# Kernel tuning notes

Hardware: AMD Instinct MI355X
Metric: run time of the kernel (lower is better)

The kernel has to match this reference:

```python
import jax, jax.numpy as jnp
import numpy as np


def setup_inputs() -> dict:
    key = jax.random.key(0)
    k1, k2 = jax.random.split(key)
    x = jax.random.normal(k1, (8, 2500, 100), dtype=jnp.float32)          # [B, L, E]
    label_feature = jax.random.normal(k2, (8922, 100), dtype=jnp.float32)  # [N, E]
    return {"x": x, "label_feature": label_feature}


def reference(x, label_feature):
    # scores: [B, N, L] = label_feature @ x^T (broadcast query over batch), unscaled
    scores = jnp.einsum("ne,ble->bnl", label_feature, x)
    alpha = jax.nn.softmax(scores, axis=2)  # softmax over sequence length
    # m: [B, N, E] = alpha @ x
    m = jnp.einsum("bnl,ble->bne", alpha, x)
    return m
```

## Files before the change

### kernel.cpp

```cpp
#include <hip/hip_runtime.h>
#include <math.h>
#include <stdint.h>

typedef __attribute__((ext_vector_type(8))) _Float16 half8;
typedef __attribute__((ext_vector_type(4))) _Float16 half4;
typedef __attribute__((ext_vector_type(4))) float f32x4;

constexpr int Bb = 8, Ll = 2500, Ee = 100, Nn = 8922;
constexpr int LP = 2560, EP = 128, NP = 8960;
constexpr int LT = 64;
constexpr int NTILES = LP / LT;
constexpr int NTB = 128;

constexpr size_t SZ_LF = (size_t)NP * EP * 2;
constexpr size_t SZ_XW = (size_t)Bb * LP * EP * 2;
constexpr size_t OFF_XW = SZ_LF;
constexpr size_t OFF_XT = OFF_XW + SZ_XW;
constexpr size_t WS_NEED = OFF_XT + SZ_XW;

__device__ __forceinline__ void gload16(const void* g, void* l) {
    __builtin_amdgcn_global_load_lds(
        (const __attribute__((address_space(1))) uint32_t*)g,
        (__attribute__((address_space(3))) uint32_t*)l, 16, 0, 0);
}

__global__ __launch_bounds__(256)
void prep_lf(const float* __restrict__ lf, uint32_t* __restrict__ dst) {
    int idx = blockIdx.x * 256 + threadIdx.x;
    int n = idx >> 6, ep = idx & 63;
    int e0 = 2 * ep, e1 = e0 + 1;
    float f0 = (n < Nn && e0 < Ee) ? lf[(size_t)n * Ee + e0] : 0.f;
    float f1 = (n < Nn && e1 < Ee) ? lf[(size_t)n * Ee + e1] : (e1 == 127 ? 1.0f : 0.f);
    union { _Float16 h[2]; uint32_t u; } cv;
    cv.h[0] = (_Float16)f0; cv.h[1] = (_Float16)f1;
    dst[idx] = cv.u;
}

__global__ __launch_bounds__(256)
void prep_x(const float* __restrict__ x, uint32_t* __restrict__ dxw,
            uint16_t* __restrict__ dxt) {
    __shared__ float lx[LT][101];
    const int l0 = blockIdx.x * LT;
    const int b  = blockIdx.y;
    for (int i = threadIdx.x; i < LT * Ee; i += 256) {
        int ll = i / Ee, e = i - ll * Ee;
        int l = l0 + ll;
        lx[ll][e] = (l < Ll) ? x[((size_t)b * Ll + l) * Ee + e] : 0.f;
    }
    __syncthreads();
    for (int i = threadIdx.x; i < LT * 64; i += 256) {
        int row = i >> 6, ep = i & 63;
        int l = l0 + row;
        int e0 = 2 * ep, e1 = e0 + 1;
        float f0 = (e0 < Ee) ? lx[row][e0] : 0.f;
        float f1;
        if (e1 < Ee)        f1 = lx[row][e1];
        else if (e1 == 127) f1 = (l < Ll) ? 0.f : -20000.f;
        else                f1 = 0.f;
        union { _Float16 h[2]; uint32_t u; } cv;
        cv.h[0] = (_Float16)f0; cv.h[1] = (_Float16)f1;
        int boff = (4 * ep) ^ ((row & 7) << 4);
        dxw[((size_t)b * LP + l) * 64 + (boff >> 2)] = cv.u;
    }
    for (int i = threadIdx.x; i < EP * LT; i += 256) {
        int e = i >> 6, ll = i & 63;
        float v = (e < Ee) ? lx[ll][e] : 0.f;
        uint32_t boff = (uint32_t)((2 * ll) ^ ((e & 7) << 4));
        union { _Float16 h; uint16_t u; } cv; cv.h = (_Float16)v;
        dxt[((size_t)b * EP + e) * LP + l0 + (boff >> 1)] = cv.u;
    }
}

__global__ __launch_bounds__(256, 2)
void cwa_mfma(const uint16_t* __restrict__ lf16, const uint16_t* __restrict__ xw,
              const uint16_t* __restrict__ xt, float* __restrict__ out) {
    __shared__ __align__(128) char smem[2 * 32768 + 4 * 4096];
    const int tid = threadIdx.x, lane = tid & 63, w = tid >> 6;
    const int g = lane >> 4, nl = lane & 15;
    const int b = blockIdx.y;
    const int n_base = blockIdx.x * NTB + w * 32;

    half8 qf[2][4];
#pragma unroll
    for (int nh = 0; nh < 2; nh++) {
        const uint16_t* qr = lf16 + (size_t)(n_base + 16 * nh + nl) * EP + 8 * g;
#pragma unroll
        for (int ks = 0; ks < 4; ks++) qf[nh][ks] = *(const half8*)(qr + 32 * ks);
    }

    f32x4 oacc[2][7];
#pragma unroll
    for (int nh = 0; nh < 2; nh++)
#pragma unroll
        for (int es = 0; es < 7; es++) oacc[nh][es] = f32x4{0.f, 0.f, 0.f, 0.f};
    float m_i[2] = {-INFINITY, -INFINITY}, s_i[2] = {0.f, 0.f};

    const char* xwb = (const char*)(xw + (size_t)b * LP * EP);
    const char* xtb = (const char*)(xt + (size_t)b * EP * LP);

    auto stage = [&](int t, char* kbuf) {
        const char* kg = xwb + (size_t)t * LT * EP * 2;
        const char* vg = xtb + (size_t)t * LT * 2;
        char* vbuf = kbuf + 16384;
#pragma unroll
        for (int i = 0; i < 4; i++) {
            int uo = i * 4096 + w * 1024;
            gload16(kg + uo + lane * 16, kbuf + uo);
        }
#pragma unroll
        for (int i = 0; i < 4; i++) {
            int e0 = w * 32 + i * 8;
            gload16(vg + (size_t)(e0 + (lane >> 3)) * (LP * 2) + (lane & 7) * 16,
                    vbuf + e0 * 128);
        }
    };

    stage(0, smem);
    asm volatile("s_waitcnt vmcnt(0)" ::: "memory");
    __syncthreads();

    char* pb = smem + 65536 + w * 4096;
    const int swp = (nl & 7) << 4;

    for (int t = 0; t < NTILES; t++) {
        const int buf = t & 1;
        const char* kb = smem + buf * 32768;
        const char* vb = kb + 16384;

        if (t + 1 < NTILES) stage(t + 1, smem + (buf ^ 1) * 32768);

        f32x4 sacc[2][4];
#pragma unroll
        for (int nh = 0; nh < 2; nh++)
#pragma unroll
            for (int ls = 0; ls < 4; ls++) sacc[nh][ls] = f32x4{0.f, 0.f, 0.f, 0.f};
#pragma unroll
        for (int ls = 0; ls < 4; ls++) {
            const int lrow = 16 * ls + nl;
            const char* kr = kb + lrow * 256;
            const int sw = (lrow & 7) << 4;
#pragma unroll
            for (int ks = 0; ks < 4; ks++) {
                half8 kf = *(const half8*)(kr + ((64 * ks + 16 * g) ^ sw));
                sacc[0][ls] = __builtin_amdgcn_mfma_f32_16x16x32_f16(kf, qf[0][ks], sacc[0][ls], 0, 0, 0);
                sacc[1][ls] = __builtin_amdgcn_mfma_f32_16x16x32_f16(kf, qf[1][ks], sacc[1][ls], 0, 0, 0);
            }
        }

        float scale_s[2];
        half4 ph[2][4];
#pragma unroll
        for (int nh = 0; nh < 2; nh++) {
            float tm = -INFINITY;
#pragma unroll
            for (int ls = 0; ls < 4; ls++)
#pragma unroll
                for (int r = 0; r < 4; r++) tm = fmaxf(tm, sacc[nh][ls][r]);
            tm = fmaxf(tm, __shfl_xor(tm, 16, 64));
            tm = fmaxf(tm, __shfl_xor(tm, 32, 64));
            const float mn = fmaxf(m_i[nh], tm);
            scale_s[nh] = __expf(m_i[nh] - mn);
            float ts = 0.f;
#pragma unroll
            for (int ls = 0; ls < 4; ls++)
#pragma unroll
                for (int r = 0; r < 4; r++) {
                    float pv = __expf(sacc[nh][ls][r] - mn);
                    ts += pv;
                    ph[nh][ls][r] = (_Float16)pv;
                }
            ts += __shfl_xor(ts, 16, 64);
            ts += __shfl_xor(ts, 32, 64);
            s_i[nh] = s_i[nh] * scale_s[nh] + ts;
            m_i[nh] = mn;
        }

#pragma unroll
        for (int nh = 0; nh < 2; nh++)
#pragma unroll
            for (int r = 0; r < 4; r++) {
                float scr = __shfl(scale_s[nh], 4 * g + r, 64);
#pragma unroll
                for (int es = 0; es < 7; es++) oacc[nh][es][r] *= scr;
            }

#pragma unroll
        for (int nh = 0; nh < 2; nh++)
#pragma unroll
            for (int ls = 0; ls < 4; ls++)
                *(half4*)(pb + (16 * nh + nl) * 128 + ((32 * ls + 8 * g) ^ swp)) = ph[nh][ls];

#pragma unroll
        for (int kl = 0; kl < 2; kl++) {
            half8 pf0 = *(const half8*)(pb + nl * 128 + ((64 * kl + 16 * g) ^ swp));
            half8 pf1 = *(const half8*)(pb + (16 + nl) * 128 + ((64 * kl + 16 * g) ^ swp));
#pragma unroll
            for (int es = 0; es < 7; es++) {
                const int er = 16 * es + nl;
                half8 vf = *(const half8*)(vb + er * 128 + ((64 * kl + 16 * g) ^ ((er & 7) << 4)));
                oacc[0][es] = __builtin_amdgcn_mfma_f32_16x16x32_f16(pf0, vf, oacc[0][es], 0, 0, 0);
                oacc[1][es] = __builtin_amdgcn_mfma_f32_16x16x32_f16(pf1, vf, oacc[1][es], 0, 0, 0);
            }
        }

        asm volatile("s_waitcnt vmcnt(0)" ::: "memory");
        __syncthreads();
    }

#pragma unroll
    for (int nh = 0; nh < 2; nh++) {
        const float inv = 1.0f / s_i[nh];
#pragma unroll
        for (int r = 0; r < 4; r++) {
            const float invr = __shfl(inv, 4 * g + r, 64);
            const int n = n_base + 16 * nh + 4 * g + r;
            if (n < Nn) {
#pragma unroll
                for (int es = 0; es < 7; es++) {
                    const int e = 16 * es + nl;
                    if (e < Ee) out[((size_t)b * Nn + n) * Ee + e] = oacc[nh][es][r] * invr;
                }
            }
        }
    }
}

constexpr int FNT = 16, FLT = 64, FLTP = 65;
__global__ __launch_bounds__(256)
void cwa_fwd(const float* __restrict__ x, const float* __restrict__ lf,
             float* __restrict__ out) {
    __shared__ float q[FNT][Ee];
    __shared__ float xts[Ee][FLTP];
    __shared__ float pl[FNT][FLT];
    const int tid = threadIdx.x, lane = tid & 63, w = tid >> 6;
    const int b = blockIdx.y, n0 = blockIdx.x * FNT;
    for (int idx = tid; idx < FNT * Ee; idx += 256) {
        int nl = idx / Ee, e = idx - nl * Ee;
        int n = n0 + nl;
        q[nl][e] = (n < Nn) ? lf[n * Ee + e] : 0.0f;
    }
    float m_i[4], s_i[4], a0[4], a1[4];
#pragma unroll
    for (int i = 0; i < 4; i++) { m_i[i] = -INFINITY; s_i[i] = 0.f; a0[i] = 0.f; a1[i] = 0.f; }
    const float* xb = x + (size_t)b * Ll * Ee;
    const bool hi_ok = lane < (Ee - 64);
    for (int l0 = 0; l0 < Ll; l0 += FLT) {
        const int nrows = min(FLT, Ll - l0);
        __syncthreads();
        for (int idx = tid; idx < FLT * (Ee / 4); idx += 256) {
            int r = idx / (Ee / 4), c4 = idx - r * (Ee / 4);
            float4 v = make_float4(0.f, 0.f, 0.f, 0.f);
            if (r < nrows) v = *reinterpret_cast<const float4*>(xb + (size_t)(l0 + r) * Ee + c4 * 4);
            xts[c4 * 4 + 0][r] = v.x; xts[c4 * 4 + 1][r] = v.y;
            xts[c4 * 4 + 2][r] = v.z; xts[c4 * 4 + 3][r] = v.w;
        }
        __syncthreads();
        float sc[4] = {0.f, 0.f, 0.f, 0.f};
        for (int e = 0; e < Ee; e++) {
            float xv = xts[e][lane];
#pragma unroll
            for (int i = 0; i < 4; i++) sc[i] = fmaf(q[4 * w + i][e], xv, sc[i]);
        }
        const bool valid = lane < nrows;
#pragma unroll
        for (int i = 0; i < 4; i++) {
            float s = valid ? sc[i] : -INFINITY;
            float tm = s;
#pragma unroll
            for (int msk = 32; msk >= 1; msk >>= 1) tm = fmaxf(tm, __shfl_xor(tm, msk, 64));
            float mn = fmaxf(m_i[i], tm);
            float p = __expf(s - mn);
            float sm = p;
#pragma unroll
            for (int msk = 32; msk >= 1; msk >>= 1) sm += __shfl_xor(sm, msk, 64);
            float scl = __expf(m_i[i] - mn);
            s_i[i] = s_i[i] * scl + sm; m_i[i] = mn;
            a0[i] *= scl; a1[i] *= scl;
            pl[4 * w + i][lane] = p;
        }
        __syncthreads();
#pragma unroll 4
        for (int l = 0; l < FLT; l++) {
            float xv0 = xts[lane][l];
            float xv1 = hi_ok ? xts[64 + lane][l] : 0.f;
#pragma unroll
            for (int i = 0; i < 4; i++) {
                float pv = pl[4 * w + i][l];
                a0[i] = fmaf(pv, xv0, a0[i]); a1[i] = fmaf(pv, xv1, a1[i]);
            }
        }
    }
#pragma unroll
    for (int i = 0; i < 4; i++) {
        int n = n0 + 4 * w + i;
        if (n >= Nn) continue;
        float inv = 1.0f / s_i[i];
        size_t base = ((size_t)b * Nn + n) * Ee;
        out[base + lane] = a0[i] * inv;
        if (hi_ok) out[base + 64 + lane] = a1[i] * inv;
    }
}

extern "C" void kernel_launch(void* const* d_in, const int* in_sizes, int n_in,
                              void* d_out, int out_size, void* d_ws, size_t ws_size,
                              hipStream_t stream) {
    const float* x  = (const float*)d_in[0];
    const float* lf = (const float*)d_in[1];
    float* out = (float*)d_out;
    if (ws_size >= WS_NEED) {
        prep_lf<<<NP * 64 / 256, 256, 0, stream>>>(lf, (uint32_t*)d_ws);
        prep_x<<<dim3(LP / LT, Bb), 256, 0, stream>>>(
            x, (uint32_t*)((char*)d_ws + OFF_XW), (uint16_t*)((char*)d_ws + OFF_XT));
        cwa_mfma<<<dim3(NP / NTB, Bb), 256, 0, stream>>>(
            (const uint16_t*)d_ws, (const uint16_t*)((char*)d_ws + OFF_XW),
            (const uint16_t*)((char*)d_ws + OFF_XT), out);
    } else {
        dim3 grid((Nn + FNT - 1) / FNT, Bb);
        cwa_fwd<<<grid, dim3(256), 0, stream>>>(x, lf, out);
    }
}
```

Baseline: 248.3 us.

## Shrink L tile to 32, raise occupancy, and add lazy softmax rescaling

Halves the sequence tile in the flash-style attention kernel, shrinking shared memory from about 80KB to 40KB and raising the launch-bounds occupancy hint from 2 to 4 blocks per CU. The V-transpose swizzle and the P scratch layout are reworked for 64-byte rows. Online softmax now rescales the accumulators only when some wave's new max exceeds the running max by more than 8, which skips most rescale work. In exchange there are twice as many loop iterations and barriers, fewer MFMAs per tile to hide latency, and a register cap that could cause spills.

```diff
diff --git a/kernel.cpp b/kernel.cpp
--- a/kernel.cpp
+++ b/kernel.cpp
@@ -8,7 +8,7 @@
 
 constexpr int Bb = 8, Ll = 2500, Ee = 100, Nn = 8922;
 constexpr int LP = 2560, EP = 128, NP = 8960;
-constexpr int LT = 64;
+constexpr int LT = 32;
 constexpr int NTILES = LP / LT;
 constexpr int NTB = 128;
 
@@ -39,16 +39,16 @@
 __global__ __launch_bounds__(256)
 void prep_x(const float* __restrict__ x, uint32_t* __restrict__ dxw,
             uint16_t* __restrict__ dxt) {
-    __shared__ float lx[LT][101];
-    const int l0 = blockIdx.x * LT;
+    __shared__ float lx[64][101];
+    const int l0 = blockIdx.x * 64;
     const int b  = blockIdx.y;
-    for (int i = threadIdx.x; i < LT * Ee; i += 256) {
+    for (int i = threadIdx.x; i < 64 * Ee; i += 256) {
         int ll = i / Ee, e = i - ll * Ee;
         int l = l0 + ll;
         lx[ll][e] = (l < Ll) ? x[((size_t)b * Ll + l) * Ee + e] : 0.f;
     }
     __syncthreads();
-    for (int i = threadIdx.x; i < LT * 64; i += 256) {
+    for (int i = threadIdx.x; i < 64 * 64; i += 256) {
         int row = i >> 6, ep = i & 63;
         int l = l0 + row;
         int e0 = 2 * ep, e1 = e0 + 1;
@@ -62,19 +62,19 @@
         int boff = (4 * ep) ^ ((row & 7) << 4);
         dxw[((size_t)b * LP + l) * 64 + (boff >> 2)] = cv.u;
     }
-    for (int i = threadIdx.x; i < EP * LT; i += 256) {
+    for (int i = threadIdx.x; i < EP * 64; i += 256) {
         int e = i >> 6, ll = i & 63;
         float v = (e < Ee) ? lx[ll][e] : 0.f;
-        uint32_t boff = (uint32_t)((2 * ll) ^ ((e & 7) << 4));
+        uint32_t boff = (uint32_t)((2 * ll) ^ ((e & 3) << 4));
         union { _Float16 h; uint16_t u; } cv; cv.h = (_Float16)v;
         dxt[((size_t)b * EP + e) * LP + l0 + (boff >> 1)] = cv.u;
     }
 }
 
-__global__ __launch_bounds__(256, 2)
+__global__ __launch_bounds__(256, 4)
 void cwa_mfma(const uint16_t* __restrict__ lf16, const uint16_t* __restrict__ xw,
               const uint16_t* __restrict__ xt, float* __restrict__ out) {
-    __shared__ __align__(128) char smem[2 * 32768 + 4 * 4096];
+    __shared__ __align__(128) char smem[16384 + 16384 + 8192];
     const int tid = threadIdx.x, lane = tid & 63, w = tid >> 6;
     const int g = lane >> 4, nl = lane & 15;
     const int b = blockIdx.y;
@@ -98,44 +98,45 @@
     const char* xwb = (const char*)(xw + (size_t)b * LP * EP);
     const char* xtb = (const char*)(xt + (size_t)b * EP * LP);
 
-    auto stage = [&](int t, char* kbuf) {
+    auto stage = [&](int t, int par) {
+        char* kbuf = smem + par * 8192;
+        char* vbuf = smem + 16384 + par * 8192;
         const char* kg = xwb + (size_t)t * LT * EP * 2;
         const char* vg = xtb + (size_t)t * LT * 2;
-        char* vbuf = kbuf + 16384;
-#pragma unroll
-        for (int i = 0; i < 4; i++) {
-            int uo = i * 4096 + w * 1024;
-            gload16(kg + uo + lane * 16, kbuf + uo);
-        }
-#pragma unroll
-        for (int i = 0; i < 4; i++) {
-            int e0 = w * 32 + i * 8;
-            gload16(vg + (size_t)(e0 + (lane >> 3)) * (LP * 2) + (lane & 7) * 16,
-                    vbuf + e0 * 128);
+#pragma unroll
+        for (int i = 0; i < 2; i++) {
+            int off = i * 4096 + w * 1024 + lane * 16;
+            gload16(kg + off, kbuf + off);
+        }
+#pragma unroll
+        for (int i = 0; i < 2; i++) {
+            int erow = i * 64 + w * 16 + (lane >> 2);
+            gload16(vg + (size_t)erow * (LP * 2) + (lane & 3) * 16,
+                    vbuf + i * 4096 + w * 1024 + lane * 16);
         }
     };
 
-    stage(0, smem);
+    stage(0, 0);
     asm volatile("s_waitcnt vmcnt(0)" ::: "memory");
     __syncthreads();
 
-    char* pb = smem + 65536 + w * 4096;
-    const int swp = (nl & 7) << 4;
+    char* pb = smem + 32768 + w * 2048;
+    const int swp = (nl & 3) << 4;
 
     for (int t = 0; t < NTILES; t++) {
-        const int buf = t & 1;
-        const char* kb = smem + buf * 32768;
-        const char* vb = kb + 16384;
-
-        if (t + 1 < NTILES) stage(t + 1, smem + (buf ^ 1) * 32768);
-
-        f32x4 sacc[2][4];
+        const int par = t & 1;
+        const char* kb = smem + par * 8192;
+        const char* vb = smem + 16384 + par * 8192;
+
+        if (t + 1 < NTILES) stage(t + 1, par ^ 1);
+
+        f32x4 sacc[2][2];
 #pragma unroll
         for (int nh = 0; nh < 2; nh++)
 #pragma unroll
-            for (int ls = 0; ls < 4; ls++) sacc[nh][ls] = f32x4{0.f, 0.f, 0.f, 0.f};
-#pragma unroll
-        for (int ls = 0; ls < 4; ls++) {
+            for (int ls = 0; ls < 2; ls++) sacc[nh][ls] = f32x4{0.f, 0.f, 0.f, 0.f};
+#pragma unroll
+        for (int ls = 0; ls < 2; ls++) {
             const int lrow = 16 * ls + nl;
             const char* kr = kb + lrow * 256;
             const int sw = (lrow & 7) << 4;
@@ -147,57 +148,62 @@
             }
         }
 
-        float scale_s[2];
-        half4 ph[2][4];
+        float tm[2];
 #pragma unroll
         for (int nh = 0; nh < 2; nh++) {
-            float tm = -INFINITY;
-#pragma unroll
-            for (int ls = 0; ls < 4; ls++)
-#pragma unroll
-                for (int r = 0; r < 4; r++) tm = fmaxf(tm, sacc[nh][ls][r]);
-            tm = fmaxf(tm, __shfl_xor(tm, 16, 64));
-            tm = fmaxf(tm, __shfl_xor(tm, 32, 64));
-            const float mn = fmaxf(m_i[nh], tm);
-            scale_s[nh] = __expf(m_i[nh] - mn);
+            float a0 = fmaxf(fmaxf(sacc[nh][0][0], sacc[nh][0][1]),
+                             fmaxf(sacc[nh][0][2], sacc[nh][0][3]));
+            float a1 = fmaxf(fmaxf(sacc[nh][1][0], sacc[nh][1][1]),
+                             fmaxf(sacc[nh][1][2], sacc[nh][1][3]));
+            float tmv = fmaxf(a0, a1);
+            tmv = fmaxf(tmv, __shfl_xor(tmv, 16, 64));
+            tmv = fmaxf(tmv, __shfl_xor(tmv, 32, 64));
+            tm[nh] = tmv;
+        }
+
+        if (!__all((tm[0] <= m_i[0] + 8.f) && (tm[1] <= m_i[1] + 8.f))) {
+#pragma unroll
+            for (int nh = 0; nh < 2; nh++) {
+                const float mn = fmaxf(m_i[nh], tm[nh]);
+                const float sc = __expf(m_i[nh] - mn);
+                m_i[nh] = mn;
+                s_i[nh] *= sc;
+#pragma unroll
+                for (int r = 0; r < 4; r++) {
+                    float scr = __shfl(sc, 4 * g + r, 64);
+#pragma unroll
+                    for (int es = 0; es < 7; es++) oacc[nh][es][r] *= scr;
+                }
+            }
+        }
+
+#pragma unroll
+        for (int nh = 0; nh < 2; nh++) {
             float ts = 0.f;
-#pragma unroll
-            for (int ls = 0; ls < 4; ls++)
+            half4 ph[2];
+#pragma unroll
+            for (int ls = 0; ls < 2; ls++)
 #pragma unroll
                 for (int r = 0; r < 4; r++) {
-                    float pv = __expf(sacc[nh][ls][r] - mn);
+                    float pv = __expf(sacc[nh][ls][r] - m_i[nh]);
                     ts += pv;
-                    ph[nh][ls][r] = (_Float16)pv;
+                    ph[ls][r] = (_Float16)pv;
                 }
             ts += __shfl_xor(ts, 16, 64);
             ts += __shfl_xor(ts, 32, 64);
-            s_i[nh] = s_i[nh] * scale_s[nh] + ts;
-            m_i[nh] = mn;
-        }
-
-#pragma unroll
-        for (int nh = 0; nh < 2; nh++)
-#pragma unroll
-            for (int r = 0; r < 4; r++) {
-                float scr = __shfl(scale_s[nh], 4 * g + r, 64);
-#pragma unroll
-                for (int es = 0; es < 7; es++) oacc[nh][es][r] *= scr;
-            }
-
-#pragma unroll
-        for (int nh = 0; nh < 2; nh++)
-#pragma unroll
-            for (int ls = 0; ls < 4; ls++)
-                *(half4*)(pb + (16 * nh + nl) * 128 + ((32 * ls + 8 * g) ^ swp)) = ph[nh][ls];
-
-#pragma unroll
-        for (int kl = 0; kl < 2; kl++) {
-            half8 pf0 = *(const half8*)(pb + nl * 128 + ((64 * kl + 16 * g) ^ swp));
-            half8 pf1 = *(const half8*)(pb + (16 + nl) * 128 + ((64 * kl + 16 * g) ^ swp));
+            s_i[nh] += ts;
+#pragma unroll
+            for (int ls = 0; ls < 2; ls++)
+                *(half4*)(pb + (16 * nh + nl) * 64 + ((32 * ls + 8 * g) ^ swp)) = ph[ls];
+        }
+
+        {
+            half8 pf0 = *(const half8*)(pb + nl * 64 + ((16 * g) ^ swp));
+            half8 pf1 = *(const half8*)(pb + (16 + nl) * 64 + ((16 * g) ^ swp));
 #pragma unroll
             for (int es = 0; es < 7; es++) {
                 const int er = 16 * es + nl;
-                half8 vf = *(const half8*)(vb + er * 128 + ((64 * kl + 16 * g) ^ ((er & 7) << 4)));
+                half8 vf = *(const half8*)(vb + er * 64 + ((16 * g) ^ ((er & 3) << 4)));
                 oacc[0][es] = __builtin_amdgcn_mfma_f32_16x16x32_f16(pf0, vf, oacc[0][es], 0, 0, 0);
                 oacc[1][es] = __builtin_amdgcn_mfma_f32_16x16x32_f16(pf1, vf, oacc[1][es], 0, 0, 0);
             }
@@ -265,10 +271,10 @@
 #pragma unroll
         for (int i = 0; i < 4; i++) {
             float s = valid ? sc[i] : -INFINITY;
-            float tm = s;
-#pragma unroll
-            for (int msk = 32; msk >= 1; msk >>= 1) tm = fmaxf(tm, __shfl_xor(tm, msk, 64));
-            float mn = fmaxf(m_i[i], tm);
+            float tmv = s;
+#pragma unroll
+            for (int msk = 32; msk >= 1; msk >>= 1) tmv = fmaxf(tmv, __shfl_xor(tmv, msk, 64));
+            float mn = fmaxf(m_i[i], tmv);
             float p = __expf(s - mn);
             float sm = p;
 #pragma unroll
@@ -309,7 +315,7 @@
     float* out = (float*)d_out;
     if (ws_size >= WS_NEED) {
         prep_lf<<<NP * 64 / 256, 256, 0, stream>>>(lf, (uint32_t*)d_ws);
-        prep_x<<<dim3(LP / LT, Bb), 256, 0, stream>>>(
+        prep_x<<<dim3(LP / 64, Bb), 256, 0, stream>>>(
             x, (uint32_t*)((char*)d_ws + OFF_XW), (uint16_t*)((char*)d_ws + OFF_XT));
         cwa_mfma<<<dim3(NP / NTB, Bb), 256, 0, stream>>>(
             (const uint16_t*)d_ws, (const uint16_t*)((char*)d_ws + OFF_XW),
```

Measured after the change: 292.8 us. 17.9% more time.
